# Performance work log

Measured on AMD Instinct MI355X. Metric: run time of the kernel, lower is better.

The kernel has to match this reference:

```python
import jax, jax.numpy as jnp
import numpy as np

N = 50000   # nodes
D = 3       # relations
E = 800000  # edges per relation
F_IN, F_HID = 300, 128
LEAKY = 0.2

def setup_inputs() -> dict:
    key = jax.random.key(0)
    ks = jax.random.split(key, 8)
    feat = jax.random.normal(ks[0], (N, F_IN), jnp.float32)
    rows = jax.random.randint(ks[1], (D, E), 0, N, jnp.int32)
    cols = jax.random.randint(ks[2], (D, E), 0, N, jnp.int32)
    # xavier_uniform-style scales
    s1 = (6.0 / (F_IN + F_HID)) ** 0.5
    s2 = (6.0 / (F_HID + F_HID)) ** 0.5
    w1 = jax.random.uniform(ks[3], (F_IN, F_HID), jnp.float32, -s1, s1)
    w2 = jax.random.uniform(ks[4], (F_HID, F_HID), jnp.float32, -s2, s2)
    b1 = jnp.zeros((F_HID,), jnp.float32)
    b2 = jnp.zeros((F_HID,), jnp.float32)
    a_att = jnp.ones((D,), jnp.float32)
    r_att = jnp.ones((D,), jnp.float32)
    label_idx = jax.random.randint(ks[5], (1000,), 0, N, jnp.int32)
    return dict(feat=feat, w1=w1, b1=b1, w2=w2, b2=b2, a_att=a_att,
                r_att=r_att, rows=rows, cols=cols, label_idx=label_idx)

def _spmm_rownorm(r, c, x):
    # y = A_norm @ x, A in COO (r,c) with value 1, rows normalized by row degree
    deg = jax.ops.segment_sum(jnp.ones_like(r, jnp.float32), r, num_segments=N)
    inv = jnp.where(deg > 0, 1.0 / jnp.maximum(deg, 1.0), 0.0)
    msgs = inv[r][:, None] * x[c]          # [E, F] gathered, weighted messages
    return jax.ops.segment_sum(msgs, r, num_segments=N)

def _graph_conv(x, w, b, rows, cols, att):
    support = x @ w + b                     # [N, F_out]
    a = jax.nn.softmax(att)                 # softmax over relations
    out = jnp.zeros((N, w.shape[1]), support.dtype)
    for i in range(D):                      # small fixed relation count
        out = out + _spmm_rownorm(rows[i], cols[i], support) * a[i]
    out = jnp.where(out > 0, out, LEAKY * out)   # LeakyReLU(0.2)
    nrm = jnp.maximum(jnp.linalg.norm(out, axis=1, keepdims=True), 1e-12)
    return out / nrm                        # F.normalize (L2, per row)

def reference(feat, w1, b1, w2, b2, a_att, r_att, rows, cols, label_idx):
    # layer 0: a_adj (forward edges), layer 1: r_adj (transposed edges)
    x = _graph_conv(feat, w1, b1, rows, cols, a_att)
    x = _graph_conv(x, w2, b2, cols, rows, r_att)
    return x[label_idx, :]
```

## Files before the change

kernel.cpp:

```cpp
#include <hip/hip_runtime.h>
#include <hip/hip_bf16.h>

#define LEAKY_SLOPE 0.2f
#define HIST_C 85
#define HIST_THREADS 1024
#define CG 5
#define CGC 17
#define KP 320

typedef __attribute__((ext_vector_type(8))) short bf16x8;
typedef __attribute__((ext_vector_type(4))) float f32x4;

__device__ __forceinline__ unsigned short f2bf(float f) {
  __hip_bfloat16 h = __float2bfloat16(f);
  return *(unsigned short*)&h;
}
__device__ __forceinline__ float bf2f(unsigned short u) {
  return __uint_as_float(((unsigned)u) << 16);
}


__global__ __launch_bounds__(256) void k_init(int* __restrict__ z, int zn,
                                              int* __restrict__ lab, int N) {
  int i = blockIdx.x * 256 + threadIdx.x;
  if (i < zn) z[i] = 0;
  if (i < N) lab[i] = -1;
}

__global__ __launch_bounds__(256) void k_lab(const int* __restrict__ lidx,
                                             unsigned* __restrict__ bm,
                                             int* __restrict__ lab_of,
                                             const float* __restrict__ a_att,
                                             const float* __restrict__ r_att,
                                             float* __restrict__ a_soft, int L) {
  int i = blockIdx.x * 256 + threadIdx.x;
  if (i == 0) {
    float m = fmaxf(fmaxf(a_att[0], a_att[1]), a_att[2]);
    float e0 = expf(a_att[0] - m), e1 = expf(a_att[1] - m), e2 = expf(a_att[2] - m);
    float s = 1.0f / (e0 + e1 + e2);
    a_soft[0] = e0 * s; a_soft[1] = e1 * s; a_soft[2] = e2 * s;
    m = fmaxf(fmaxf(r_att[0], r_att[1]), r_att[2]);
    e0 = expf(r_att[0] - m); e1 = expf(r_att[1] - m); e2 = expf(r_att[2] - m);
    s = 1.0f / (e0 + e1 + e2);
    a_soft[3] = e0 * s; a_soft[4] = e1 * s; a_soft[5] = e2 * s;
  }
  if (i < L) {
    int n = lidx[i];
    atomicOr(&bm[n >> 5], 1u << (n & 31));
    atomicMax(&lab_of[n], i);
  }
}

__global__ __launch_bounds__(256) void k_prep(const float* __restrict__ w1,
                                              unsigned short* __restrict__ WThi,
                                              unsigned short* __restrict__ WTlo, int K) {
  int i = blockIdx.x * 256 + threadIdx.x;
  if (i >= 128 * KP) return;
  int n = i / KP, k = i - n * KP;
  float f = (k < K) ? w1[(size_t)k * 128 + n] : 0.f;
  unsigned short hi = f2bf(f);
  unsigned short lo = f2bf(f - bf2f(hi));
  WThi[i] = hi;
  WTlo[i] = lo;
}

__global__ __launch_bounds__(HIST_THREADS) void k_hist(const int* __restrict__ rows,
                                                       const int* __restrict__ cols,
                                                       const unsigned* __restrict__ bm,
                                                       int* __restrict__ deg2,
                                                       unsigned* __restrict__ flag_bm,
                                                       int* __restrict__ hcnt,
                                                       int* __restrict__ hsrc, int* __restrict__ hpack,
                                                       unsigned char* __restrict__ rank8,
                                                       unsigned* __restrict__ histc,
                                                       int N, int E, int chunk) {
  extern __shared__ unsigned sh[];
  __shared__ int s_cnt;
  int WN4 = (N + 3) >> 2;
  unsigned* hist = sh;
  int tid = threadIdx.x;
  int cidx = blockIdx.x, rel = blockIdx.y;

  for (int i = tid; i < WN4; i += HIST_THREADS) hist[i] = 0;
  if (tid == 0) s_cnt = 0;
  __syncthreads();

  int estart = cidx * chunk;
  int eend = min(estart + chunk, E);
  int rbase = (rel * HIST_C + cidx) * chunk;
  for (int e0 = estart + tid; e0 < eend; e0 += 2 * HIST_THREADS) {
    int e1 = e0 + HIST_THREADS;
    bool v1 = e1 < eend;
    int r0 = rows[rel * E + e0];
    int c0 = cols[rel * E + e0];
    int r1 = v1 ? rows[rel * E + e1] : 0;
    int c1 = v1 ? cols[rel * E + e1] : 0;
    unsigned o0 = atomicAdd(&hist[r0 >> 2], 1u << (8 * (r0 & 3)));
    rank8[rel * E + e0] = (unsigned char)((o0 >> (8 * (r0 & 3))) & 0xFFu);
    if ((bm[c0 >> 5] >> (c0 & 31)) & 1u) {
      atomicAdd(&deg2[rel * N + c0], 1);
      atomicOr(&flag_bm[r0 >> 5], 1u << (r0 & 31));
      int p = atomicAdd(&s_cnt, 1);
      hsrc[rbase + p] = r0;
      hpack[rbase + p] = (rel << 20) | c0;
    }
    if (v1) {
      unsigned o1 = atomicAdd(&hist[r1 >> 2], 1u << (8 * (r1 & 3)));
      rank8[rel * E + e1] = (unsigned char)((o1 >> (8 * (r1 & 3))) & 0xFFu);
      if ((bm[c1 >> 5] >> (c1 & 31)) & 1u) {
        atomicAdd(&deg2[rel * N + c1], 1);
        atomicOr(&flag_bm[r1 >> 5], 1u << (r1 & 31));
        int p = atomicAdd(&s_cnt, 1);
        hsrc[rbase + p] = r1;
        hpack[rbase + p] = (rel << 20) | c1;
      }
    }
  }
  __syncthreads();
  if (tid == 0) hcnt[rel * HIST_C + cidx] = s_cnt;
  unsigned* dst = &histc[(size_t)(rel * HIST_C + cidx) * WN4];
  for (int i = tid; i < WN4; i += HIST_THREADS) dst[i] = hist[i];
}

__global__ __launch_bounds__(256) void k_red_a(const unsigned* __restrict__ histc,
                                               ushort4* __restrict__ psum, int WN4) {
  int word = blockIdx.x * 256 + threadIdx.x;
  if (word >= WN4) return;
  int rc = blockIdx.y;
  int rel = rc / CG, cg = rc - rel * CG;
  size_t hb = ((size_t)rel * HIST_C + cg * CGC) * WN4 + word;
  int s0 = 0, s1 = 0, s2 = 0, s3 = 0;
#pragma unroll
  for (int i = 0; i < CGC; ++i) {
    unsigned w = histc[hb + (size_t)i * WN4];
    s0 += w & 0xFFu; s1 += (w >> 8) & 0xFFu; s2 += (w >> 16) & 0xFFu; s3 += w >> 24;
  }
  psum[(size_t)rc * WN4 + word] =
      make_ushort4((unsigned short)s0, (unsigned short)s1,
                   (unsigned short)s2, (unsigned short)s3);
}

__global__ __launch_bounds__(256) void k_red_b(const ushort4* __restrict__ psum,
                                               ushort4* __restrict__ cgb,
                                               const float* __restrict__ a_soft,
                                               float* __restrict__ inv1,
                                               int* __restrict__ rowdeg, int N, int WN4) {
  int t = blockIdx.x * 256 + threadIdx.x;
  if (t >= WN4) return;
  int run[4] = {0, 0, 0, 0};
  int d0 = 4 * t;
#pragma unroll
  for (int rel = 0; rel < 3; ++rel) {
    int start[4];
#pragma unroll
    for (int j = 0; j < 4; ++j) start[j] = run[j];
#pragma unroll
    for (int cg = 0; cg < CG; ++cg) {
      size_t idx = (size_t)(rel * CG + cg) * WN4 + t;
      ushort4 p = psum[idx];
      cgb[idx] = make_ushort4((unsigned short)run[0], (unsigned short)run[1],
                              (unsigned short)run[2], (unsigned short)run[3]);
      run[0] += p.x; run[1] += p.y; run[2] += p.z; run[3] += p.w;
    }
    float a = a_soft[rel];
#pragma unroll
    for (int j = 0; j < 4; ++j) {
      int d = d0 + j;
      if (d < N) inv1[rel * N + d] = a / (float)max(run[j] - start[j], 1);
    }
  }
#pragma unroll
  for (int j = 0; j < 4; ++j) {
    int d = d0 + j;
    if (d < N) rowdeg[d] = run[j];
  }
}

__global__ __launch_bounds__(256) void k_red_c(const unsigned* __restrict__ histc,
                                               const ushort4* __restrict__ cgb,
                                               unsigned* __restrict__ cbase_w, int WN4) {
  int word = blockIdx.x * 256 + threadIdx.x;
  if (word >= WN4) return;
  int rc = blockIdx.y;
  int rel = rc / CG, cg = rc - rel * CG;
  ushort4 b = cgb[(size_t)rc * WN4 + word];
  unsigned r0 = b.x, r1 = b.y, r2 = b.z, r3 = b.w;
  size_t hb = ((size_t)rel * HIST_C + cg * CGC) * WN4 + word;
#pragma unroll
  for (int i = 0; i < CGC; ++i) {
    unsigned w = histc[hb + (size_t)i * WN4];
    cbase_w[hb + (size_t)i * WN4] =
        (r0 & 0xFFu) | ((r1 & 0xFFu) << 8) | ((r2 & 0xFFu) << 16) | ((r3 & 0xFFu) << 24);
    r0 += w & 0xFFu; r1 += (w >> 8) & 0xFFu; r2 += (w >> 16) & 0xFFu; r3 += w >> 24;
  }
}


__global__ __launch_bounds__(256) void k_scan1(const int* __restrict__ rowdeg,
                                               int* __restrict__ row_ptr,
                                               int* __restrict__ chunk_sums, int N) {
  __shared__ int sd[256];
  int tid = threadIdx.x;
  int n0 = blockIdx.x * 1024 + tid * 4;
  int v[4];
#pragma unroll
  for (int i = 0; i < 4; ++i) {
    int n = n0 + i;
    v[i] = (n < N) ? rowdeg[n] : 0;
  }
  sd[tid] = v[0] + v[1] + v[2] + v[3];
  __syncthreads();
  for (int off = 1; off < 256; off <<= 1) {
    int t = (tid >= off) ? sd[tid - off] : 0;
    __syncthreads();
    sd[tid] += t;
    __syncthreads();
  }
  int run = tid ? sd[tid - 1] : 0;
#pragma unroll
  for (int i = 0; i < 4; ++i) {
    int n = n0 + i;
    if (n < N) row_ptr[n] = run;
    run += v[i];
  }
  if (tid == 255) chunk_sums[blockIdx.x] = sd[255];
}

__global__ __launch_bounds__(64) void k_scan2(const int* __restrict__ chunk_sums,
                                              int* __restrict__ chunk_offs,
                                              int nchunks, int* __restrict__ row_ptr, int N) {
  int lane = threadIdx.x;
  int mine = (lane < nchunks) ? chunk_sums[lane] : 0;
  int v = mine;
  for (int off = 1; off < 64; off <<= 1) {
    int t = __shfl_up(v, off, 64);
    if (lane >= off) v += t;
  }
  if (lane < nchunks) chunk_offs[lane] = v - mine;
  int total = __shfl(v, nchunks - 1, 64);
  if (lane == 0) row_ptr[N] = total;
}

__global__ __launch_bounds__(256) void k_scan3(int* __restrict__ row_ptr,
                                               const int* __restrict__ chunk_offs,
                                               const unsigned* __restrict__ flag_bm,
                                               int* __restrict__ wl, int* __restrict__ wl_cnt,
                                               int N) {
  __shared__ int s_cnt, s_base;
  int tid = threadIdx.x;
  if (tid == 0) s_cnt = 0;
  __syncthreads();
  int n = blockIdx.x * 256 + tid;
  bool f = false;
  int p = 0;
  if (n < N) {
    row_ptr[n] += chunk_offs[n >> 10];
    f = (flag_bm[n >> 5] >> (n & 31)) & 1u;
    if (f) p = atomicAdd(&s_cnt, 1);
  }
  __syncthreads();
  if (tid == 0 && s_cnt > 0) s_base = atomicAdd(wl_cnt, s_cnt);
  __syncthreads();
  if (f) wl[s_base + p] = n;
}


__global__ __launch_bounds__(256) void k_scatter(const int* __restrict__ rows,
                                                 const int* __restrict__ cols,
                                                 const int* __restrict__ row_ptr,
                                                 const unsigned char* __restrict__ cbase,
                                                 const unsigned char* __restrict__ rank8,
                                                 const unsigned* __restrict__ flag_bm,
                                                 unsigned* __restrict__ esrc,
                                                 int N, int E, int chunk) {
  int e = blockIdx.x * 256 + threadIdx.x;
  int rel = blockIdx.y;
  if (e >= E) return;
  int d = rows[rel * E + e];
  if (!((flag_bm[d >> 5] >> (d & 31)) & 1u)) return;
  int s = cols[rel * E + e];
  int NP4 = ((N + 3) >> 2) * 4;
  int c = e / chunk;
  int pos = row_ptr[d] + (int)cbase[(size_t)(rel * HIST_C + c) * NP4 + d]
          + (int)rank8[rel * E + e];
  esrc[pos] = ((unsigned)rel << 16) | (unsigned)s;
}


__global__ __launch_bounds__(256) void k_gemm1(const float* __restrict__ A,
                                               const unsigned short* __restrict__ WThi,
                                               const unsigned short* __restrict__ WTlo,
                                               const float* __restrict__ bias,
                                               unsigned short* __restrict__ outbf,
                                               int M, int K) {
  __shared__ unsigned short sAhi[64 * 64];
  __shared__ unsigned short sWhi[128 * 64], sWlo[128 * 64];
  char* pAhi = (char*)sAhi;
  char* pWhi = (char*)sWhi; char* pWlo = (char*)sWlo;
  int tid = threadIdx.x;
  int wave = tid >> 6, lane = tid & 63;
  int row0 = blockIdx.x * 64;
  f32x4 acc[8];
#pragma unroll
  for (int i = 0; i < 8; ++i) acc[i] = (f32x4){0.f, 0.f, 0.f, 0.f};

  for (int c = 0; c < 5; ++c) {
    int k0 = c * 64;
    __syncthreads();
    for (int i = tid; i < 1024; i += 256) {
      int r = i >> 4, q = i & 15;
      int gr = row0 + r, gk = k0 + q * 4;
      float4 v = make_float4(0.f, 0.f, 0.f, 0.f);
      if (gr < M && gk < K) v = *(const float4*)&A[(size_t)gr * K + gk];
      unsigned h0 = (unsigned)f2bf(v.x) | ((unsigned)f2bf(v.y) << 16);
      unsigned h1 = (unsigned)f2bf(v.z) | ((unsigned)f2bf(v.w) << 16);
      int byte = (r * 128 + q * 8) ^ ((r & 7) << 4);
      *(uint2*)(pAhi + byte) = make_uint2(h0, h1);
    }
    for (int i = tid; i < 1024; i += 256) {
      int n = i >> 3, u = i & 7;
      size_t g = (size_t)n * KP + k0 + u * 8;
      int byte = (n * 128 + u * 16) ^ ((n & 7) << 4);
      *(uint4*)(pWhi + byte) = *(const uint4*)&WThi[g];
      *(uint4*)(pWlo + byte) = *(const uint4*)&WTlo[g];
    }
    __syncthreads();
#pragma unroll
    for (int ks = 0; ks < 2; ++ks) {
      int m = wave * 16 + (lane & 15);
      int kb = ks * 32 + (lane >> 4) * 8;
      bf16x8 ahi = *(const bf16x8*)(pAhi + ((m * 128 + kb * 2) ^ ((m & 7) << 4)));
#pragma unroll
      for (int nt = 0; nt < 8; ++nt) {
        int n = nt * 16 + (lane & 15);
        int wb = (n * 128 + kb * 2) ^ ((n & 7) << 4);
        bf16x8 bhi = *(const bf16x8*)(pWhi + wb);
        bf16x8 blo = *(const bf16x8*)(pWlo + wb);
        acc[nt] = __builtin_amdgcn_mfma_f32_16x16x32_bf16(ahi, bhi, acc[nt], 0, 0, 0);
        acc[nt] = __builtin_amdgcn_mfma_f32_16x16x32_bf16(ahi, blo, acc[nt], 0, 0, 0);
      }
    }
  }
#pragma unroll
  for (int nt = 0; nt < 8; ++nt) {
    int n = nt * 16 + (lane & 15);
    float bv = bias[n];
#pragma unroll
    for (int j = 0; j < 4; ++j) {
      int m = row0 + wave * 16 + (lane >> 4) * 4 + j;
      if (m < M) outbf[(size_t)m * 128 + n] = f2bf(acc[nt][j] + bv);
    }
  }
}


__global__ __launch_bounds__(256) void k_agg_norm(const unsigned short* __restrict__ supp,
                                                  const int* __restrict__ row_ptr,
                                                  const unsigned* __restrict__ esrc,
                                                  const float* __restrict__ inv1,
                                                  const int* __restrict__ wl,
                                                  const int* __restrict__ wl_cnt,
                                                  unsigned short* __restrict__ out, int N) {
  int wi = blockIdx.x * 4 + (threadIdx.x >> 6);
  if (wi >= wl_cnt[0]) return;
  int row = __builtin_amdgcn_readfirstlane(wl[wi]);
  int lane = threadIdx.x & 63;
  int grp = lane >> 4;
  int l16 = lane & 15;
  int s = row_ptr[row], e = row_ptr[row + 1];
  float w0 = inv1[row], w1 = inv1[N + row], w2 = inv1[2 * N + row];
  float acc[8] = {};
  for (int j = s; j < e; j += 8) {
    int j0 = j + grp, j1 = j + 4 + grp;
    bool a0 = j0 < e, a1 = j1 < e;
    unsigned u0 = esrc[a0 ? j0 : s];
    unsigned u1 = esrc[a1 ? j1 : s];
    int rel0 = (int)(u0 >> 16), src0 = (int)(u0 & 0xFFFFu);
    int rel1 = (int)(u1 >> 16), src1 = (int)(u1 & 0xFFFFu);
    float wa = (rel0 == 0) ? w0 : ((rel0 == 1) ? w1 : w2);
    float wb = (rel1 == 0) ? w0 : ((rel1 == 1) ? w1 : w2);
    if (!a0) wa = 0.f;
    if (!a1) wb = 0.f;
    uint4 p0 = *(const uint4*)&supp[(size_t)src0 * 128 + l16 * 8];
    uint4 p1 = *(const uint4*)&supp[(size_t)src1 * 128 + l16 * 8];
#pragma unroll
    for (int q = 0; q < 4; ++q) {
      unsigned pa = (&p0.x)[q];
      unsigned pb = (&p1.x)[q];
      acc[2 * q]     += wa * __uint_as_float(pa << 16) + wb * __uint_as_float(pb << 16);
      acc[2 * q + 1] += wa * __uint_as_float(pa & 0xFFFF0000u) +
                        wb * __uint_as_float(pb & 0xFFFF0000u);
    }
  }
#pragma unroll
  for (int i = 0; i < 8; ++i) {
    acc[i] += __shfl_xor(acc[i], 16, 64);
    acc[i] += __shfl_xor(acc[i], 32, 64);
  }
  float ss = 0.f;
#pragma unroll
  for (int i = 0; i < 8; ++i) {
    acc[i] = acc[i] > 0.f ? acc[i] : LEAKY_SLOPE * acc[i];
    ss += acc[i] * acc[i];
  }
#pragma unroll
  for (int m = 1; m < 16; m <<= 1) ss += __shfl_xor(ss, m, 64);
  float inv = 1.0f / fmaxf(sqrtf(ss), 1e-12f);
  if (lane < 16) {
    unsigned pk[4];
#pragma unroll
    for (int q = 0; q < 4; ++q) {
      pk[q] = (unsigned)f2bf(acc[2 * q] * inv) |
              ((unsigned)f2bf(acc[2 * q + 1] * inv) << 16);
    }
    *(uint4*)&out[(size_t)row * 128 + l16 * 8] = make_uint4(pk[0], pk[1], pk[2], pk[3]);
  }
}

__global__ __launch_bounds__(1024) void k_cnt2(const int* __restrict__ lidx,
                                               const int* __restrict__ lab_of,
                                               const int* __restrict__ deg2,
                                               const float* __restrict__ a_soft,
                                               int* __restrict__ hb_ptr,
                                               int* __restrict__ cnt2,
                                               int* __restrict__ fill2,
                                               float* __restrict__ sumw, int N, int L) {
  __shared__ int sd[1024];
  int t = threadIdx.x;
  int cnt = 0;
  if (t < L) {
    int d = lidx[t];
    int c0 = deg2[d], c1 = deg2[N + d], c2 = deg2[2 * N + d];
    if (lab_of[d] == t) cnt = c0 + c1 + c2;
    sumw[t] = a_soft[3] * (c0 > 0 ? 1.f : 0.f) +
              a_soft[4] * (c1 > 0 ? 1.f : 0.f) +
              a_soft[5] * (c2 > 0 ? 1.f : 0.f);
  }
  sd[t] = cnt;
  __syncthreads();
  for (int off = 1; off < 1024; off <<= 1) {
    int v = (t >= off) ? sd[t - off] : 0;
    __syncthreads();
    sd[t] += v;
    __syncthreads();
  }
  if (t < L) {
    int base = sd[t] - cnt;
    hb_ptr[t] = base;
    fill2[t] = base;
    cnt2[t] = cnt;
  }
}

__global__ __launch_bounds__(256) void k_scatter2(const int* __restrict__ hsrc,
                                                  const int* __restrict__ hpack,
                                                  const int* __restrict__ hcnt,
                                                  const int* __restrict__ lab_of,
                                                  int* __restrict__ fill2,
                                                  unsigned* __restrict__ hdata, int chunk) {
  int reg = blockIdx.x;
  int cnt = hcnt[reg];
  int rbase = reg * chunk;
  for (int i = threadIdx.x; i < cnt; i += 256) {
    int src = hsrc[rbase + i], pk = hpack[rbase + i];
    int rel = pk >> 20, d = pk & 0xFFFFF;
    int li = lab_of[d];
    int pos = atomicAdd(&fill2[li], 1);
    hdata[pos] = ((unsigned)rel << 16) | (unsigned)src;
  }
}

__global__ __launch_bounds__(256) void k_agg2(const unsigned short* __restrict__ h1,
                                              const int* __restrict__ hb_ptr,
                                              const int* __restrict__ cnt2,
                                              const unsigned* __restrict__ hdata,
                                              const int* __restrict__ lidx,
                                              const int* __restrict__ deg2,
                                              const float* __restrict__ a_soft,
                                              float* __restrict__ aggh, int N, int L) {
  int wv = blockIdx.x * 4 + (threadIdx.x >> 6);
  if (wv >= L) return;
  int li = __builtin_amdgcn_readfirstlane(wv);
  int lane = threadIdx.x & 63;
  int grp = lane >> 4, l16 = lane & 15;
  int d = lidx[li];
  int s = hb_ptr[li], e = s + cnt2[li];
  float w0 = a_soft[3] / (float)max(deg2[d], 1);
  float w1 = a_soft[4] / (float)max(deg2[N + d], 1);
  float w2 = a_soft[5] / (float)max(deg2[2 * N + d], 1);
  float acc[8] = {};
  for (int j = s; j < e; j += 4) {
    int jj = j + grp;
    bool act = jj < e;
    unsigned u = hdata[act ? jj : s];
    int rel = (int)(u >> 16);
    int src = (int)(u & 0xFFFFu);
    float w = (rel == 0) ? w0 : ((rel == 1) ? w1 : w2);
    if (!act) w = 0.f;
    uint4 pv = *(const uint4*)&h1[(size_t)src * 128 + l16 * 8];
#pragma unroll
    for (int q = 0; q < 4; ++q) {
      unsigned p = (&pv.x)[q];
      acc[2 * q]     += w * __uint_as_float(p << 16);
      acc[2 * q + 1] += w * __uint_as_float(p & 0xFFFF0000u);
    }
  }
#pragma unroll
  for (int i = 0; i < 8; ++i) {
    acc[i] += __shfl_xor(acc[i], 16, 64);
    acc[i] += __shfl_xor(acc[i], 32, 64);
  }
  if (lane < 16) {
    *(float4*)&aggh[(size_t)li * 128 + l16 * 8] =
        make_float4(acc[0], acc[1], acc[2], acc[3]);
    *(float4*)&aggh[(size_t)li * 128 + l16 * 8 + 4] =
        make_float4(acc[4], acc[5], acc[6], acc[7]);
  }
}

__global__ __launch_bounds__(256) void k_final(const float* __restrict__ aggh,
                                               const float* __restrict__ W2,
                                               const float* __restrict__ b2,
                                               const float* __restrict__ sumw,
                                               const int* __restrict__ lidx,
                                               const int* __restrict__ lab_of,
                                               float* __restrict__ out, int L) {
  __shared__ float sW[64][128];
  __shared__ float sA[32][64];
  __shared__ int s_c[32];
  __shared__ float s_sw[32];
  int tid = threadIdx.x;
  int wave = tid >> 6, lane = tid & 63;
  int lane2 = lane * 2;
  int row0 = blockIdx.x * 32;
  if (tid < 32) {
    int gr = row0 + tid;
    int c = 0; float sw = 0.f;
    if (gr < L) { c = lab_of[lidx[gr]]; sw = sumw[gr]; }
    s_c[tid] = c; s_sw[tid] = sw;
  }
  __syncthreads();
  float acc[8][2] = {};
  for (int k0 = 0; k0 < 128; k0 += 64) {
    __syncthreads();
    for (int i = tid; i < 64 * 32; i += 256) {
      int kk = i >> 5, c4 = i & 31;
      ((float4*)&sW[kk][0])[c4] = ((const float4*)&W2[(size_t)(k0 + kk) * 128])[c4];
    }
    for (int i = tid; i < 32 * 16; i += 256) {
      int r = i >> 4, kq = i & 15;
      int gr = row0 + r;
      float4 v = make_float4(0.f, 0.f, 0.f, 0.f);
      if (gr < L) v = ((const float4*)&aggh[(size_t)s_c[r] * 128 + k0])[kq];
      ((float4*)&sA[r][0])[kq] = v;
    }
    __syncthreads();
    const float* ap = &sA[wave * 8][0];
    for (int kk = 0; kk < 64; kk += 2) {
      float2 w0 = *(const float2*)&sW[kk][lane2];
      float2 w1 = *(const float2*)&sW[kk + 1][lane2];
#pragma unroll
      for (int r = 0; r < 8; ++r) {
        float2 av = *(const float2*)&ap[r * 64 + kk];
        acc[r][0] += av.x * w0.x + av.y * w1.x;
        acc[r][1] += av.x * w0.y + av.y * w1.y;
      }
    }
  }
  float2 bv = *(const float2*)&b2[lane2];
#pragma unroll
  for (int r = 0; r < 8; ++r) {
    int gr = row0 + wave * 8 + r;
    float sw = s_sw[wave * 8 + r];
    float ax = acc[r][0] + bv.x * sw;
    float ay = acc[r][1] + bv.y * sw;
    ax = ax > 0.f ? ax : LEAKY_SLOPE * ax;
    ay = ay > 0.f ? ay : LEAKY_SLOPE * ay;
    float ss = ax * ax + ay * ay;
#pragma unroll
    for (int m = 1; m < 64; m <<= 1) ss += __shfl_xor(ss, m, 64);
    float inv = 1.0f / fmaxf(sqrtf(ss), 1e-12f);
    if (gr < L) {
      *(float2*)&out[(size_t)gr * 128 + lane2] = make_float2(ax * inv, ay * inv);
    }
  }
}


extern "C" void kernel_launch(void* const* d_in, const int* in_sizes, int n_in,
                              void* d_out, int out_size, void* d_ws, size_t ws_size,
                              hipStream_t stream) {
  const float* feat  = (const float*)d_in[0];
  const float* w1    = (const float*)d_in[1];
  const float* b1    = (const float*)d_in[2];
  const float* w2    = (const float*)d_in[3];
  const float* b2    = (const float*)d_in[4];
  const float* a_att = (const float*)d_in[5];
  const float* r_att = (const float*)d_in[6];
  const int* rows    = (const int*)d_in[7];
  const int* cols    = (const int*)d_in[8];
  const int* lidx    = (const int*)d_in[9];

  const int F = 128;
  int K1 = in_sizes[1] / F;
  int N  = in_sizes[0] / K1;
  int E  = in_sizes[7] / 3;
  int L  = in_sizes[9];
  float* outp = (float*)d_out;
  (void)n_in; (void)out_size; (void)ws_size;

  int WN4 = (N + 3) >> 2;
  int chunk = (E + HIST_C - 1) / HIST_C;

  char* base = (char*)d_ws;
  size_t off = 0;
  auto take = [&](size_t bytes) -> void* {
    size_t cur = (off + 255) & ~(size_t)255;
    off = cur + bytes;
    return (void*)(base + cur);
  };
  unsigned short* suppbf = (unsigned short*)take((size_t)N * F * 2);
  unsigned short* h1 = (unsigned short*)take((size_t)N * F * 2);
  unsigned* esrc = (unsigned*)take((size_t)3 * E * 4);
  unsigned char* rank8 = (unsigned char*)take((size_t)3 * E);
  unsigned* histc = (unsigned*)take((size_t)3 * HIST_C * WN4 * 4);
  unsigned* cbase_w = (unsigned*)take((size_t)3 * HIST_C * WN4 * 4);
  ushort4* psum = (ushort4*)take((size_t)15 * WN4 * 8);
  ushort4* cgb  = (ushort4*)take((size_t)15 * WN4 * 8);
  float* inv1  = (float*)take((size_t)3 * N * 4);
  int* rowdeg  = (int*)take((size_t)N * 4);
  int* row_ptr = (int*)take((size_t)(N + 1) * 4);
  int* wl      = (int*)take((size_t)N * 4);
  int* hsrc  = (int*)take((size_t)3 * HIST_C * chunk * 4);
  int* hpack = (int*)take((size_t)3 * HIST_C * chunk * 4);
  unsigned short* WThi = (unsigned short*)take((size_t)128 * KP * 2);
  unsigned short* WTlo = (unsigned short*)take((size_t)128 * KP * 2);
  float* aggh = (float*)take((size_t)1024 * F * 4);
  int* lab_of = (int*)take((size_t)N * 4);
  int nb = (N + 31) / 32;
  int zn = 3 * N + 2 * nb + 1;
  int* deg2 = (int*)take((size_t)zn * 4);
  unsigned* bm = (unsigned*)(deg2 + 3 * N);
  unsigned* flag_bm = bm + nb;
  int* wl_cnt = (int*)(flag_bm + nb);
  int* hcnt = (int*)take((size_t)(3 * HIST_C + 1) * 4);
  int* hb_ptr = (int*)take(1024 * 4);
  int* cnt2   = (int*)take(1024 * 4);
  int* fill2  = (int*)take(1024 * 4);
  float* sumw = (float*)take(1024 * 4);
  float* a_soft = (float*)take(64);
  int* chunk_sums = (int*)take(256);
  int* chunk_offs = (int*)take(256);
  unsigned* hdata = esrc;

  int nchunks = (N + 1023) / 1024;
  int nwb = (WN4 + 255) / 256;
  size_t shbytes = (size_t)WN4 * 4;
  hipFuncSetAttribute((const void*)k_hist, hipFuncAttributeMaxDynamicSharedMemorySize,
                      (int)shbytes);

  hipLaunchKernelGGL(k_init, dim3((max(zn, N) + 255) / 256), dim3(256), 0, stream,
                     deg2, zn, lab_of, N);
  hipLaunchKernelGGL(k_lab, dim3((L + 255) / 256), dim3(256), 0, stream,
                     lidx, bm, lab_of, a_att, r_att, a_soft, L);
  hipLaunchKernelGGL(k_prep, dim3((128 * KP + 255) / 256), dim3(256), 0, stream,
                     w1, WThi, WTlo, K1);
  hipLaunchKernelGGL(k_hist, dim3(HIST_C, 3), dim3(HIST_THREADS), shbytes, stream,
                     rows, cols, bm, deg2, flag_bm, hcnt, hsrc, hpack, rank8, histc,
                     N, E, chunk);
  hipLaunchKernelGGL(k_gemm1, dim3((N + 63) / 64), dim3(256), 0, stream,
                     feat, WThi, WTlo, b1, suppbf, N, K1);
  hipLaunchKernelGGL(k_red_a, dim3(nwb, 15), dim3(256), 0, stream, histc, psum, WN4);
  hipLaunchKernelGGL(k_red_b, dim3(nwb), dim3(256), 0, stream,
                     psum, cgb, a_soft, inv1, rowdeg, N, WN4);
  hipLaunchKernelGGL(k_red_c, dim3(nwb, 15), dim3(256), 0, stream, histc, cgb, cbase_w, WN4);
  hipLaunchKernelGGL(k_scan1, dim3(nchunks), dim3(256), 0, stream, rowdeg, row_ptr, chunk_sums, N);
  hipLaunchKernelGGL(k_scan2, dim3(1), dim3(64), 0, stream, chunk_sums, chunk_offs, nchunks, row_ptr, N);
  hipLaunchKernelGGL(k_scan3, dim3((N + 255) / 256), dim3(256), 0, stream,
                     row_ptr, chunk_offs, flag_bm, wl, wl_cnt, N);
  hipLaunchKernelGGL(k_scatter, dim3((E + 255) / 256, 3), dim3(256), 0, stream,
                     rows, cols, row_ptr, (const unsigned char*)cbase_w, rank8, flag_bm,
                     esrc, N, E, chunk);
  hipLaunchKernelGGL(k_agg_norm, dim3((N + 3) / 4), dim3(256), 0, stream,
                     suppbf, row_ptr, esrc, inv1, wl, wl_cnt, h1, N);
  hipLaunchKernelGGL(k_cnt2, dim3(1), dim3(1024), 0, stream,
                     lidx, lab_of, deg2, a_soft, hb_ptr, cnt2, fill2, sumw, N, L);
  hipLaunchKernelGGL(k_scatter2, dim3(3 * HIST_C), dim3(256), 0, stream,
                     hsrc, hpack, hcnt, lab_of, fill2, hdata, chunk);
  hipLaunchKernelGGL(k_agg2, dim3((L + 3) / 4), dim3(256), 0, stream,
                     h1, hb_ptr, cnt2, hdata, lidx, deg2, a_soft, aggh, N, L);
  hipLaunchKernelGGL(k_final, dim3((L + 31) / 32), dim3(256), 0, stream,
                     aggh, w2, b2, sumw, lidx, lab_of, outp, L);
}
```

Measured before the change: 234.1 us.

## Vectorize histogram and scatter edge loads, switch layer-1 support to fp16 dot2

```diff
diff --git a/kernel.cpp b/kernel.cpp
--- a/kernel.cpp
+++ b/kernel.cpp
@@ -1,5 +1,6 @@
 #include <hip/hip_runtime.h>
 #include <hip/hip_bf16.h>
+#include <hip/hip_fp16.h>
 
 #define LEAKY_SLOPE 0.2f
 #define HIST_C 85
@@ -10,6 +11,7 @@
 
 typedef __attribute__((ext_vector_type(8))) short bf16x8;
 typedef __attribute__((ext_vector_type(4))) float f32x4;
+typedef _Float16 h2 __attribute__((ext_vector_type(2)));
 
 __device__ __forceinline__ unsigned short f2bf(float f) {
   __hip_bfloat16 h = __float2bfloat16(f);
@@ -17,6 +19,10 @@
 }
 __device__ __forceinline__ float bf2f(unsigned short u) {
   return __uint_as_float(((unsigned)u) << 16);
+}
+__device__ __forceinline__ unsigned short f2h(float f) {
+  __half h = __float2half(f);
+  return *(unsigned short*)&h;
 }
 
 
@@ -88,31 +94,50 @@
   int estart = cidx * chunk;
   int eend = min(estart + chunk, E);
   int rbase = (rel * HIST_C + cidx) * chunk;
-  for (int e0 = estart + tid; e0 < eend; e0 += 2 * HIST_THREADS) {
-    int e1 = e0 + HIST_THREADS;
-    bool v1 = e1 < eend;
-    int r0 = rows[rel * E + e0];
-    int c0 = cols[rel * E + e0];
-    int r1 = v1 ? rows[rel * E + e1] : 0;
-    int c1 = v1 ? cols[rel * E + e1] : 0;
-    unsigned o0 = atomicAdd(&hist[r0 >> 2], 1u << (8 * (r0 & 3)));
-    rank8[rel * E + e0] = (unsigned char)((o0 >> (8 * (r0 & 3))) & 0xFFu);
-    if ((bm[c0 >> 5] >> (c0 & 31)) & 1u) {
-      atomicAdd(&deg2[rel * N + c0], 1);
-      atomicOr(&flag_bm[r0 >> 5], 1u << (r0 & 31));
-      int p = atomicAdd(&s_cnt, 1);
-      hsrc[rbase + p] = r0;
-      hpack[rbase + p] = (rel << 20) | c0;
-    }
-    if (v1) {
-      unsigned o1 = atomicAdd(&hist[r1 >> 2], 1u << (8 * (r1 & 3)));
-      rank8[rel * E + e1] = (unsigned char)((o1 >> (8 * (r1 & 3))) & 0xFFu);
-      if ((bm[c1 >> 5] >> (c1 & 31)) & 1u) {
-        atomicAdd(&deg2[rel * N + c1], 1);
-        atomicOr(&flag_bm[r1 >> 5], 1u << (r1 & 31));
-        int p = atomicAdd(&s_cnt, 1);
-        hsrc[rbase + p] = r1;
-        hpack[rbase + p] = (rel << 20) | c1;
+  const int* rp = rows + (size_t)rel * E;
+  const int* cp = cols + (size_t)rel * E;
+  for (int base = estart + tid * 8; base < eend; base += 8 * HIST_THREADS) {
+    int r[8], c[8];
+    bool full = (base + 7) < eend;
+    if (full) {
+      *(int4*)&r[0] = *(const int4*)&rp[base];
+      *(int4*)&r[4] = *(const int4*)&rp[base + 4];
+      *(int4*)&c[0] = *(const int4*)&cp[base];
+      *(int4*)&c[4] = *(const int4*)&cp[base + 4];
+    } else {
+#pragma unroll
+      for (int j = 0; j < 8; ++j) {
+        int e = base + j;
+        r[j] = (e < eend) ? rp[e] : 0;
+        c[j] = (e < eend) ? cp[e] : 0;
+      }
+    }
+    unsigned rk0 = 0, rk1 = 0;
+#pragma unroll
+    for (int j = 0; j < 8; ++j) {
+      if (base + j < eend) {
+        int rj = r[j], cj = c[j];
+        unsigned old = atomicAdd(&hist[rj >> 2], 1u << (8 * (rj & 3)));
+        unsigned rv = (old >> (8 * (rj & 3))) & 0xFFu;
+        if (j < 4) rk0 |= rv << (8 * j); else rk1 |= rv << (8 * (j - 4));
+        if ((bm[cj >> 5] >> (cj & 31)) & 1u) {
+          atomicAdd(&deg2[rel * N + cj], 1);
+          atomicOr(&flag_bm[rj >> 5], 1u << (rj & 31));
+          int p = atomicAdd(&s_cnt, 1);
+          hsrc[rbase + p] = rj;
+          hpack[rbase + p] = (rel << 20) | cj;
+        }
+      }
+    }
+    if (full) {
+      *(uint2*)&rank8[(size_t)rel * E + base] = make_uint2(rk0, rk1);
+    } else {
+#pragma unroll
+      for (int j = 0; j < 8; ++j) {
+        if (base + j < eend) {
+          unsigned rv = (j < 4) ? (rk0 >> (8 * j)) : (rk1 >> (8 * (j - 4)));
+          rank8[(size_t)rel * E + base + j] = (unsigned char)(rv & 0xFFu);
+        }
       }
     }
   }
@@ -273,17 +298,40 @@
                                                  const unsigned* __restrict__ flag_bm,
                                                  unsigned* __restrict__ esrc,
                                                  int N, int E, int chunk) {
-  int e = blockIdx.x * 256 + threadIdx.x;
+  int e0 = (blockIdx.x * 256 + threadIdx.x) * 4;
   int rel = blockIdx.y;
-  if (e >= E) return;
-  int d = rows[rel * E + e];
-  if (!((flag_bm[d >> 5] >> (d & 31)) & 1u)) return;
-  int s = cols[rel * E + e];
+  if (e0 >= E) return;
+  const int* rp = rows + (size_t)rel * E;
+  const int* cp = cols + (size_t)rel * E;
+  int r[4], c[4];
+  unsigned rk;
+  if (e0 + 3 < E) {
+    *(int4*)r = *(const int4*)&rp[e0];
+    *(int4*)c = *(const int4*)&cp[e0];
+    rk = *(const unsigned*)&rank8[(size_t)rel * E + e0];
+  } else {
+    rk = 0;
+#pragma unroll
+    for (int j = 0; j < 4; ++j) {
+      int e = e0 + j;
+      r[j] = (e < E) ? rp[e] : 0;
+      c[j] = (e < E) ? cp[e] : 0;
+      if (e < E) rk |= (unsigned)rank8[(size_t)rel * E + e] << (8 * j);
+    }
+  }
   int NP4 = ((N + 3) >> 2) * 4;
-  int c = e / chunk;
-  int pos = row_ptr[d] + (int)cbase[(size_t)(rel * HIST_C + c) * NP4 + d]
-          + (int)rank8[rel * E + e];
-  esrc[pos] = ((unsigned)rel << 16) | (unsigned)s;
+  int c0 = e0 / chunk;
+  int rem = e0 - c0 * chunk;
+#pragma unroll
+  for (int j = 0; j < 4; ++j) {
+    if (e0 + j >= E) break;
+    int d = r[j];
+    if (!((flag_bm[d >> 5] >> (d & 31)) & 1u)) continue;
+    int cch = (rem + j >= chunk) ? c0 + 1 : c0;
+    int pos = row_ptr[d] + (int)cbase[(size_t)(rel * HIST_C + cch) * NP4 + d]
+            + (int)((rk >> (8 * j)) & 0xFFu);
+    esrc[pos] = ((unsigned)rel << 16) | (unsigned)c[j];
+  }
 }
 
 
@@ -291,7 +339,7 @@
                                                const unsigned short* __restrict__ WThi,
                                                const unsigned short* __restrict__ WTlo,
                                                const float* __restrict__ bias,
-                                               unsigned short* __restrict__ outbf,
+                                               unsigned short* __restrict__ outh,
                                                int M, int K) {
   __shared__ unsigned short sAhi[64 * 64];
   __shared__ unsigned short sWhi[128 * 64], sWlo[128 * 64];
@@ -348,7 +396,7 @@
 #pragma unroll
     for (int j = 0; j < 4; ++j) {
       int m = row0 + wave * 16 + (lane >> 4) * 4 + j;
-      if (m < M) outbf[(size_t)m * 128 + n] = f2bf(acc[nt][j] + bv);
+      if (m < M) outh[(size_t)m * 128 + n] = f2h(acc[nt][j] + bv);
     }
   }
 }
@@ -368,7 +416,9 @@
   int grp = lane >> 4;
   int l16 = lane & 15;
   int s = row_ptr[row], e = row_ptr[row + 1];
-  float w0 = inv1[row], w1 = inv1[N + row], w2 = inv1[2 * N + row];
+  _Float16 w0h = (_Float16)inv1[row];
+  _Float16 w1h = (_Float16)inv1[N + row];
+  _Float16 w2h = (_Float16)inv1[2 * N + row];
   float acc[8] = {};
   for (int j = s; j < e; j += 8) {
     int j0 = j + grp, j1 = j + 4 + grp;
@@ -377,19 +427,24 @@
     unsigned u1 = esrc[a1 ? j1 : s];
     int rel0 = (int)(u0 >> 16), src0 = (int)(u0 & 0xFFFFu);
     int rel1 = (int)(u1 >> 16), src1 = (int)(u1 & 0xFFFFu);
-    float wa = (rel0 == 0) ? w0 : ((rel0 == 1) ? w1 : w2);
-    float wb = (rel1 == 0) ? w0 : ((rel1 == 1) ? w1 : w2);
-    if (!a0) wa = 0.f;
-    if (!a1) wb = 0.f;
+    _Float16 wa = (rel0 == 0) ? w0h : ((rel0 == 1) ? w1h : w2h);
+    _Float16 wb = (rel1 == 0) ? w0h : ((rel1 == 1) ? w1h : w2h);
+    if (!a0) wa = (_Float16)0.f;
+    if (!a1) wb = (_Float16)0.f;
+    h2 wpk;
+    wpk[0] = wa; wpk[1] = wb;
     uint4 p0 = *(const uint4*)&supp[(size_t)src0 * 128 + l16 * 8];
     uint4 p1 = *(const uint4*)&supp[(size_t)src1 * 128 + l16 * 8];
 #pragma unroll
     for (int q = 0; q < 4; ++q) {
-      unsigned pa = (&p0.x)[q];
-      unsigned pb = (&p1.x)[q];
-      acc[2 * q]     += wa * __uint_as_float(pa << 16) + wb * __uint_as_float(pb << 16);
-      acc[2 * q + 1] += wa * __uint_as_float(pa & 0xFFFF0000u) +
-                        wb * __uint_as_float(pb & 0xFFFF0000u);
+      unsigned a = (&p0.x)[q];
+      unsigned b = (&p1.x)[q];
+      unsigned lo = __builtin_amdgcn_perm(b, a, 0x05040100u);
+      unsigned hi = __builtin_amdgcn_perm(b, a, 0x07060302u);
+      acc[2 * q]     = __builtin_amdgcn_fdot2(__builtin_bit_cast(h2, lo), wpk,
+                                              acc[2 * q], false);
+      acc[2 * q + 1] = __builtin_amdgcn_fdot2(__builtin_bit_cast(h2, hi), wpk,
+                                              acc[2 * q + 1], false);
     }
   }
 #pragma unroll
@@ -610,7 +665,7 @@
   (void)n_in; (void)out_size; (void)ws_size;
 
   int WN4 = (N + 3) >> 2;
-  int chunk = (E + HIST_C - 1) / HIST_C;
+  int chunk = (((E + HIST_C - 1) / HIST_C) + 7) & ~7;
 
   char* base = (char*)d_ws;
   size_t off = 0;
@@ -619,7 +674,7 @@
     off = cur + bytes;
     return (void*)(base + cur);
   };
-  unsigned short* suppbf = (unsigned short*)take((size_t)N * F * 2);
+  unsigned short* supph = (unsigned short*)take((size_t)N * F * 2);
   unsigned short* h1 = (unsigned short*)take((size_t)N * F * 2);
   unsigned* esrc = (unsigned*)take((size_t)3 * E * 4);
   unsigned char* rank8 = (unsigned char*)take((size_t)3 * E);
@@ -669,7 +724,7 @@
                      rows, cols, bm, deg2, flag_bm, hcnt, hsrc, hpack, rank8, histc,
                      N, E, chunk);
   hipLaunchKernelGGL(k_gemm1, dim3((N + 63) / 64), dim3(256), 0, stream,
-                     feat, WThi, WTlo, b1, suppbf, N, K1);
+                     feat, WThi, WTlo, b1, supph, N, K1);
   hipLaunchKernelGGL(k_red_a, dim3(nwb, 15), dim3(256), 0, stream, histc, psum, WN4);
   hipLaunchKernelGGL(k_red_b, dim3(nwb), dim3(256), 0, stream,
                      psum, cgb, a_soft, inv1, rowdeg, N, WN4);
@@ -678,11 +733,11 @@
   hipLaunchKernelGGL(k_scan2, dim3(1), dim3(64), 0, stream, chunk_sums, chunk_offs, nchunks, row_ptr, N);
   hipLaunchKernelGGL(k_scan3, dim3((N + 255) / 256), dim3(256), 0, stream,
                      row_ptr, chunk_offs, flag_bm, wl, wl_cnt, N);
-  hipLaunchKernelGGL(k_scatter, dim3((E + 255) / 256, 3), dim3(256), 0, stream,
+  hipLaunchKernelGGL(k_scatter, dim3((E + 1023) / 1024, 3), dim3(256), 0, stream,
                      rows, cols, row_ptr, (const unsigned char*)cbase_w, rank8, flag_bm,
                      esrc, N, E, chunk);
   hipLaunchKernelGGL(k_agg_norm, dim3((N + 3) / 4), dim3(256), 0, stream,
-                     suppbf, row_ptr, esrc, inv1, wl, wl_cnt, h1, N);
+                     supph, row_ptr, esrc, inv1, wl, wl_cnt, h1, N);
   hipLaunchKernelGGL(k_cnt2, dim3(1), dim3(1024), 0, stream,
                      lidx, lab_of, deg2, a_soft, hb_ptr, cnt2, fill2, sumw, N, L);
   hipLaunchKernelGGL(k_scatter2, dim3(3 * HIST_C), dim3(256), 0, stream,
```

After: 241.4 us. +3.1%, slower.
